# Optimization experiments

Hardware: AMD Instinct MI355X
Metric: run time of the kernel (lower is better)

The kernel has to match this reference:

```python
import jax, jax.numpy as jnp
import numpy as np

HEAD_SIZE = 1024
NUM_HEADS = 8
D_K = HEAD_SIZE // NUM_HEADS  # only used as the softmax scale; no head split in this module
B, S = 8, 2048


def setup_inputs() -> dict:
    key = jax.random.key(0)
    ks = jax.random.split(key, 11)
    d = HEAD_SIZE
    scale = 1.0 / np.sqrt(d)
    inp = {
        'query': jax.random.normal(ks[0], (B, S, d), dtype=jnp.float32),
        'key': jax.random.normal(ks[1], (B, S, d), dtype=jnp.float32),
        'value': jax.random.normal(ks[2], (B, S, d), dtype=jnp.float32),
        'Wq': jax.random.normal(ks[3], (d, d), dtype=jnp.float32) * scale,
        'bq': jnp.zeros((d,), dtype=jnp.float32),
        'Wk': jax.random.normal(ks[4], (d, d), dtype=jnp.float32) * scale,
        'bk': jnp.zeros((d,), dtype=jnp.float32),
        'Wv': jax.random.normal(ks[5], (d, d), dtype=jnp.float32) * scale,
        'bv': jnp.zeros((d,), dtype=jnp.float32),
        'Wo': jax.random.normal(ks[6], (d, d), dtype=jnp.float32) * scale,
        'bo': jnp.zeros((d,), dtype=jnp.float32),
    }
    return inp


def reference(query, key, value, Wq, bq, Wk, bk, Wv, bv, Wo, bo):
    # per-input linear projections (torch Linear: x @ W.T + b)
    q = jnp.einsum('bsd,ed->bse', query, Wq) + bq
    k = jnp.einsum('bsd,ed->bse', key, Wk) + bk
    v = jnp.einsum('bsd,ed->bse', value, Wv) + bv
    # NOTE: no head split in the original module; scale uses d_k = head_size/num_heads
    scores = jnp.einsum('bqd,bkd->bqk', q, k) / jnp.sqrt(jnp.float32(D_K))
    p_attn = jax.nn.softmax(scores, axis=-1)  # [B, S, S]
    x = jnp.einsum('bqk,bkd->bqd', p_attn, v)
    out = jnp.einsum('bsd,ed->bse', x, Wo) + bo
    return out
```

## Files before the change

### kernel.cpp

```cpp
#include <hip/hip_runtime.h>
#include <hip/hip_bf16.h>
#include <math.h>

typedef __bf16 bf16_t;
typedef _Float16 f16_t;
typedef bf16_t bf16x8 __attribute__((ext_vector_type(8)));
typedef bf16_t bf16x4 __attribute__((ext_vector_type(4)));
typedef f16_t  f16x8  __attribute__((ext_vector_type(8)));
typedef f16_t  f16x4  __attribute__((ext_vector_type(4)));
typedef float  f32x4  __attribute__((ext_vector_type(4)));

__global__ __launch_bounds__(256) void cvt_f32_bf16(
    const float* __restrict__ in, bf16_t* __restrict__ out, int n4) {
  int i = blockIdx.x * 256 + threadIdx.x;
  if (i >= n4) return;
  float4 v = ((const float4*)in)[i];
  bf16x4 o;
  o[0] = (bf16_t)v.x; o[1] = (bf16_t)v.y; o[2] = (bf16_t)v.z; o[3] = (bf16_t)v.w;
  ((bf16x4*)out)[i] = o;
}

__global__ __launch_bounds__(256) void transpose_bf16(
    const bf16_t* __restrict__ in, bf16_t* __restrict__ out, int R, int C) {
  __shared__ bf16_t t[64][65];
  size_t boff = (size_t)blockIdx.z * R * C;
  in += boff; out += boff;
  int r0 = blockIdx.y * 64, c0 = blockIdx.x * 64;
  int x = threadIdx.x & 63, y4 = threadIdx.x >> 6;
  #pragma unroll
  for (int yy = y4; yy < 64; yy += 4)
    t[yy][x] = in[(size_t)(r0 + yy) * C + c0 + x];
  __syncthreads();
  #pragma unroll
  for (int yy = y4; yy < 64; yy += 4)
    out[(size_t)(c0 + yy) * R + r0 + x] = t[x][yy];
}

__global__ __launch_bounds__(256) void softmax_rows_f16(f16_t* __restrict__ sc) {
  f16_t* rp = sc + (size_t)blockIdx.x * 2048;
  int tid = threadIdx.x;
  f16x8 v = ((const f16x8*)rp)[tid];
  float f[8];
  #pragma unroll
  for (int t = 0; t < 8; t++) f[t] = (float)v[t];

  float m = f[0];
  #pragma unroll
  for (int t = 1; t < 8; t++) m = fmaxf(m, f[t]);
  #pragma unroll
  for (int o = 32; o; o >>= 1) m = fmaxf(m, __shfl_xor(m, o));
  __shared__ float redm[4];
  if ((tid & 63) == 0) redm[tid >> 6] = m;
  __syncthreads();
  m = fmaxf(fmaxf(redm[0], redm[1]), fmaxf(redm[2], redm[3]));

  float s = 0.f;
  #pragma unroll
  for (int t = 0; t < 8; t++) { f[t] = __expf(f[t] - m); s += f[t]; }
  #pragma unroll
  for (int o = 32; o; o >>= 1) s += __shfl_xor(s, o);
  __shared__ float reds[4];
  if ((tid & 63) == 0) reds[tid >> 6] = s;
  __syncthreads();
  s = reds[0] + reds[1] + reds[2] + reds[3];
  float inv = 1.0f / s;

  bf16x8 o8;
  #pragma unroll
  for (int t = 0; t < 8; t++) o8[t] = (bf16_t)(f[t] * inv);
  ((bf16x8*)rp)[tid] = o8;
}

__device__ __forceinline__ void store4(float* p, float4 v) { *(float4*)p = v; }
__device__ __forceinline__ void store4(bf16_t* p, float4 v) {
  bf16x4 o; o[0] = (bf16_t)v.x; o[1] = (bf16_t)v.y;
  o[2] = (bf16_t)v.z; o[3] = (bf16_t)v.w; *(bf16x4*)p = o;
}
__device__ __forceinline__ void store4(f16_t* p, float4 v) {
  f16x4 o; o[0] = (f16_t)v.x; o[1] = (f16_t)v.y;
  o[2] = (f16_t)v.z; o[3] = (f16_t)v.w; *(f16x4*)p = o;
}

#define BM 256
#define BN 256
#define BK 64

__device__ __forceinline__ void load16_lds(const bf16_t* g, bf16_t* l) {
  __builtin_amdgcn_global_load_lds(
      (__attribute__((address_space(1))) void*)const_cast<bf16_t*>(g),
      (__attribute__((address_space(3))) void*)l, 16, 0, 0);
}

template <typename CT>
__global__ __launch_bounds__(512, 2) void gemm256(
    const bf16_t* __restrict__ A, int lda, size_t strA,
    const bf16_t* __restrict__ B, int ldb, size_t strB,
    CT* __restrict__ C, int ldc, size_t strC,
    const float* __restrict__ bias, float scale,
    int K, int batch_on_x) {
  __shared__ __align__(16) char smem[2][65536];

  int bz, mt, nt;
  if (batch_on_x) { bz = blockIdx.x; nt = blockIdx.y; mt = blockIdx.z; }
  else            { mt = blockIdx.x; nt = blockIdx.y; bz = blockIdx.z; }
  A += (size_t)bz * strA;
  B += (size_t)bz * strB;
  C += (size_t)bz * strC;
  int m0 = mt * BM, n0 = nt * BN;
  int tid  = threadIdx.x;
  int lane = tid & 63, wv = tid >> 6;
  int wrow = wv >> 2;
  int wcol = wv & 3;

  f32x4 acc[8][4];
  #pragma unroll
  for (int i = 0; i < 8; i++)
    #pragma unroll
    for (int j = 0; j < 4; j++) acc[i][j] = (f32x4)0.f;

  int lrow = lane & 15;
  int lk8  = (lane >> 4) * 8;
  int xm   = (lrow & 8) << 2;

  auto rd = [&](const char* base, int blk16, int kcol) -> bf16x8 {
    int byte = (((blk16 << 1) + (kcol >> 5)) << 10)
             + (lrow << 6) + (((kcol & 31) << 1) ^ xm);
    return *(const bf16x8*)(base + byte);
  };

  auto stage_half = [&](int h) {
    int th = h >> 2, hf = h & 3;
    char* dstb = smem[th & 1] + hf * 16384;
    const bf16_t* g; int rb, ld;
    if (hf < 2) { g = A; rb = m0 + hf * 128;       ld = lda; }
    else        { g = B; rb = n0 + (hf - 2) * 128; ld = ldb; }
    int k0 = th * BK;
    #pragma unroll
    for (int q = 0; q < 2; q++) {
      int l = q * 8192 + wv * 1024 + lane * 16;
      int inner = l & 1023, s = l >> 10;
      int rl   = ((s >> 1) << 4) | (inner >> 6);
      int colb = (inner & 63) ^ (((inner >> 9) & 1) << 5);
      int col  = ((s & 1) << 5) | (colb >> 1);
      load16_lds(g + (size_t)(rb + rl) * ld + k0 + col,
                 (bf16_t*)(dstb + q * 8192 + wv * 1024));
    }
  };

  int nk = K / BK;

  #pragma unroll
  for (int h = 0; h < 6; ++h)
    if (h < 4 * nk) stage_half(h);
  asm volatile("s_waitcnt vmcnt(4)" ::: "memory");
  asm volatile("s_barrier" ::: "memory");

  bf16x8 a0[4][2], a1[4][2], bb[2][2];

  for (int t = 0; t < nk; ++t) {
    const char* Ab = smem[t & 1];
    const char* Bb = smem[t & 1] + 32768;
    int hb = 4 * t + 6;

    #pragma unroll
    for (int i = 0; i < 4; ++i)
      #pragma unroll
      for (int s = 0; s < 2; ++s)
        a0[i][s] = rd(Ab, wrow * 8 + i, s * 32 + lk8);
    #pragma unroll
    for (int j = 0; j < 2; ++j)
      #pragma unroll
      for (int s = 0; s < 2; ++s)
        bb[j][s] = rd(Bb, wcol * 4 + j, s * 32 + lk8);
    if (hb + 0 < 4 * nk) stage_half(hb + 0);
    asm volatile("s_barrier" ::: "memory");
    asm volatile("s_waitcnt lgkmcnt(0)");
    __builtin_amdgcn_s_setprio(1);
    #pragma unroll
    for (int i = 0; i < 4; ++i)
      #pragma unroll
      for (int j = 0; j < 2; ++j)
        #pragma unroll
        for (int s = 0; s < 2; ++s)
          acc[i][j] = __builtin_amdgcn_mfma_f32_16x16x32_bf16(
              a0[i][s], bb[j][s], acc[i][j], 0, 0, 0);
    __builtin_amdgcn_s_setprio(0);
    asm volatile("s_barrier" ::: "memory");

    #pragma unroll
    for (int i = 0; i < 4; ++i)
      #pragma unroll
      for (int s = 0; s < 2; ++s)
        a1[i][s] = rd(Ab, wrow * 8 + 4 + i, s * 32 + lk8);
    if (hb + 1 < 4 * nk) stage_half(hb + 1);
    asm volatile("s_barrier" ::: "memory");
    asm volatile("s_waitcnt lgkmcnt(0)");
    __builtin_amdgcn_s_setprio(1);
    #pragma unroll
    for (int i = 0; i < 4; ++i)
      #pragma unroll
      for (int j = 0; j < 2; ++j)
        #pragma unroll
        for (int s = 0; s < 2; ++s)
          acc[4 + i][j] = __builtin_amdgcn_mfma_f32_16x16x32_bf16(
              a1[i][s], bb[j][s], acc[4 + i][j], 0, 0, 0);
    __builtin_amdgcn_s_setprio(0);
    asm volatile("s_barrier" ::: "memory");

    #pragma unroll
    for (int j = 0; j < 2; ++j)
      #pragma unroll
      for (int s = 0; s < 2; ++s)
        bb[j][s] = rd(Bb, wcol * 4 + 2 + j, s * 32 + lk8);
    if (hb + 2 < 4 * nk) stage_half(hb + 2);
    asm volatile("s_barrier" ::: "memory");
    asm volatile("s_waitcnt lgkmcnt(0)");
    __builtin_amdgcn_s_setprio(1);
    #pragma unroll
    for (int i = 0; i < 4; ++i)
      #pragma unroll
      for (int j = 0; j < 2; ++j)
        #pragma unroll
        for (int s = 0; s < 2; ++s)
          acc[4 + i][2 + j] = __builtin_amdgcn_mfma_f32_16x16x32_bf16(
              a1[i][s], bb[j][s], acc[4 + i][2 + j], 0, 0, 0);
    __builtin_amdgcn_s_setprio(0);
    asm volatile("s_barrier" ::: "memory");

    if (hb + 3 < 4 * nk) stage_half(hb + 3);
    asm volatile("s_barrier" ::: "memory");
    __builtin_amdgcn_s_setprio(1);
    #pragma unroll
    for (int i = 0; i < 4; ++i)
      #pragma unroll
      for (int j = 0; j < 2; ++j)
        #pragma unroll
        for (int s = 0; s < 2; ++s)
          acc[i][2 + j] = __builtin_amdgcn_mfma_f32_16x16x32_bf16(
              a0[i][s], bb[j][s], acc[i][2 + j], 0, 0, 0);
    __builtin_amdgcn_s_setprio(0);
    if (t < nk - 2) asm volatile("s_waitcnt vmcnt(4)" ::: "memory");
    else            asm volatile("s_waitcnt vmcnt(0)" ::: "memory");
    asm volatile("s_barrier" ::: "memory");
  }

  float* Cs = (float*)smem[0];
  #pragma unroll
  for (int q = 0; q < 4; ++q) {
    __syncthreads();
    if (wrow == (q >> 1)) {
      #pragma unroll
      for (int ii = 0; ii < 4; ++ii) {
        int i = (q & 1) * 4 + ii;
        int lr = ii * 16 + (lane >> 4) * 4;
        #pragma unroll
        for (int j = 0; j < 4; ++j) {
          int lc = wcol * 64 + j * 16 + (lane & 15);
          #pragma unroll
          for (int r = 0; r < 4; ++r)
            Cs[(lr + r) * 260 + lc] = acc[i][j][r];
        }
      }
    }
    __syncthreads();
    #pragma unroll
    for (int io = 0; io < 8; ++io) {
      int idx = io * 512 + tid;
      int r = idx >> 6, c4 = (idx & 63) * 4;
      float4 v = *(const float4*)&Cs[r * 260 + c4];
      int grow = m0 + q * 64 + r;
      int gcol = n0 + c4;
      float4 bv = bias ? *(const float4*)&bias[gcol] : make_float4(0, 0, 0, 0);
      v.x = v.x * scale + bv.x; v.y = v.y * scale + bv.y;
      v.z = v.z * scale + bv.z; v.w = v.w * scale + bv.w;
      store4(C + (size_t)grow * ldc + gcol, v);
    }
  }
}

extern "C" void kernel_launch(void* const* d_in, const int* in_sizes, int n_in,
                              void* d_out, int out_size, void* d_ws, size_t ws_size,
                              hipStream_t stream) {
  const float* query = (const float*)d_in[0];
  const float* key_  = (const float*)d_in[1];
  const float* value = (const float*)d_in[2];
  const float* Wq = (const float*)d_in[3];
  const float* bq = (const float*)d_in[4];
  const float* Wk = (const float*)d_in[5];
  const float* bk = (const float*)d_in[6];
  const float* Wv = (const float*)d_in[7];
  const float* bv = (const float*)d_in[8];
  const float* Wo = (const float*)d_in[9];
  const float* bo = (const float*)d_in[10];
  float* out = (float*)d_out;

  const int Bb = 8, S = 2048, D = 1024;
  const int MS = Bb * S;
  const size_t ND = (size_t)MS * D;
  const size_t WD = (size_t)D * D;

  char* ws = (char*)d_ws;
  bf16_t* Wqb = (bf16_t*)ws;
  bf16_t* Wkb = Wqb + WD;
  bf16_t* Wvb = Wkb + WD;
  bf16_t* Wob = Wvb + WD;
  f16_t*  SC  = (f16_t*)(Wob + WD);
  bf16_t* IN  = (bf16_t*)SC;
  bf16_t* Qb  = (bf16_t*)((char*)SC + (size_t)Bb * S * S * 2);
  bf16_t* Kb  = Qb + ND;
  bf16_t* VT  = Kb;
  bf16_t* Xb  = Kb + ND;

  const int n4i = (int)(ND / 4), n4w = (int)(WD / 4);
  dim3 blk(512);

  cvt_f32_bf16<<<dim3(n4w / 256), 256, 0, stream>>>(Wq, Wqb, n4w);
  cvt_f32_bf16<<<dim3(n4w / 256), 256, 0, stream>>>(Wk, Wkb, n4w);
  cvt_f32_bf16<<<dim3(n4w / 256), 256, 0, stream>>>(Wv, Wvb, n4w);
  cvt_f32_bf16<<<dim3(n4w / 256), 256, 0, stream>>>(Wo, Wob, n4w);

  dim3 pgrid(MS / BM, D / BN, 1);
  cvt_f32_bf16<<<dim3(n4i / 256), 256, 0, stream>>>(query, IN, n4i);
  gemm256<bf16_t><<<pgrid, blk, 0, stream>>>(
      IN, D, 0, Wqb, D, 0, Qb, D, 0, bq, 1.f, D, 0);
  cvt_f32_bf16<<<dim3(n4i / 256), 256, 0, stream>>>(key_, IN, n4i);
  gemm256<bf16_t><<<pgrid, blk, 0, stream>>>(
      IN, D, 0, Wkb, D, 0, Kb, D, 0, bk, 1.f, D, 0);
  cvt_f32_bf16<<<dim3(n4i / 256), 256, 0, stream>>>(value, IN, n4i);
  gemm256<bf16_t><<<pgrid, blk, 0, stream>>>(
      IN, D, 0, Wvb, D, 0, Xb, D, 0, bv, 1.f, D, 0);

  gemm256<f16_t><<<dim3(Bb, S / BN, S / BM), blk, 0, stream>>>(
      Qb, D, (size_t)S * D, Kb, D, (size_t)S * D, SC, S, (size_t)S * S,
      nullptr, 0.08838834764831845f, D, 1);

  transpose_bf16<<<dim3(D / 64, S / 64, Bb), 256, 0, stream>>>(Xb, VT, S, D);

  softmax_rows_f16<<<dim3(Bb * S), 256, 0, stream>>>(SC);

  gemm256<bf16_t><<<dim3(Bb, D / BN, S / BM), blk, 0, stream>>>(
      (const bf16_t*)SC, S, (size_t)S * S, VT, S, (size_t)D * S,
      Xb, D, (size_t)S * D, nullptr, 1.f, S, 1);

  gemm256<float><<<pgrid, blk, 0, stream>>>(
      Xb, D, 0, Wob, D, 0, out, D, 0, bo, 1.f, D, 0);
}
```

Baseline: 574.3 us.

## Replace double-buffered LDS with a 10-slot ring to deepen global prefetch

```diff
diff --git a/kernel.cpp b/kernel.cpp
--- a/kernel.cpp
+++ b/kernel.cpp
@@ -98,7 +98,8 @@
     CT* __restrict__ C, int ldc, size_t strC,
     const float* __restrict__ bias, float scale,
     int K, int batch_on_x) {
-  __shared__ __align__(16) char smem[2][65536];
+  __shared__ __align__(16) char smem[10][16384];
+  char* smem0 = &smem[0][0];
 
   int bz, mt, nt;
   if (batch_on_x) { bz = blockIdx.x; nt = blockIdx.y; mt = blockIdx.z; }
@@ -122,15 +123,15 @@
   int lk8  = (lane >> 4) * 8;
   int xm   = (lrow & 8) << 2;
 
-  auto rd = [&](const char* base, int blk16, int kcol) -> bf16x8 {
-    int byte = (((blk16 << 1) + (kcol >> 5)) << 10)
+  auto rd = [&](const char* half, int blk, int kcol) -> bf16x8 {
+    int byte = (((blk << 1) + (kcol >> 5)) << 10)
              + (lrow << 6) + (((kcol & 31) << 1) ^ xm);
-    return *(const bf16x8*)(base + byte);
+    return *(const bf16x8*)(half + byte);
   };
 
-  auto stage_half = [&](int h) {
+  auto stage_half = [&](int h, int slot) {
     int th = h >> 2, hf = h & 3;
-    char* dstb = smem[th & 1] + hf * 16384;
+    char* dstb = smem0 + slot * 16384;
     const bf16_t* g; int rb, ld;
     if (hf < 2) { g = A; rb = m0 + hf * 128;       ld = lda; }
     else        { g = B; rb = n0 + (hf - 2) * 128; ld = ldb; }
@@ -148,31 +149,37 @@
   };
 
   int nk = K / BK;
-
-  #pragma unroll
-  for (int h = 0; h < 6; ++h)
-    if (h < 4 * nk) stage_half(h);
-  asm volatile("s_waitcnt vmcnt(4)" ::: "memory");
+  int nh = 4 * nk;
+
+  #pragma unroll
+  for (int h = 0; h < 8; ++h)
+    if (h < nh) stage_half(h, h);
+  asm volatile("s_waitcnt vmcnt(8)" ::: "memory");
   asm volatile("s_barrier" ::: "memory");
 
   bf16x8 a0[4][2], a1[4][2], bb[2][2];
+  int rs = 0;
+  int ss = 8;
 
   for (int t = 0; t < nk; ++t) {
-    const char* Ab = smem[t & 1];
-    const char* Bb = smem[t & 1] + 32768;
-    int hb = 4 * t + 6;
+    int hb = 4 * t + 8;
+    int sa = rs + wrow;
+    int sb = rs + 2 + (wcol >> 1); if (sb >= 10) sb -= 10;
+    const char* Ah = smem0 + sa * 16384;
+    const char* Bh = smem0 + sb * 16384;
+    int bl = (wcol & 1) * 4;
 
     #pragma unroll
     for (int i = 0; i < 4; ++i)
       #pragma unroll
       for (int s = 0; s < 2; ++s)
-        a0[i][s] = rd(Ab, wrow * 8 + i, s * 32 + lk8);
+        a0[i][s] = rd(Ah, i, s * 32 + lk8);
     #pragma unroll
     for (int j = 0; j < 2; ++j)
       #pragma unroll
       for (int s = 0; s < 2; ++s)
-        bb[j][s] = rd(Bb, wcol * 4 + j, s * 32 + lk8);
-    if (hb + 0 < 4 * nk) stage_half(hb + 0);
+        bb[j][s] = rd(Bh, bl + j, s * 32 + lk8);
+    if (hb + 0 < nh) { stage_half(hb + 0, ss); ss = (ss == 9) ? 0 : ss + 1; }
     asm volatile("s_barrier" ::: "memory");
     asm volatile("s_waitcnt lgkmcnt(0)");
     __builtin_amdgcn_s_setprio(1);
@@ -191,8 +198,8 @@
     for (int i = 0; i < 4; ++i)
       #pragma unroll
       for (int s = 0; s < 2; ++s)
-        a1[i][s] = rd(Ab, wrow * 8 + 4 + i, s * 32 + lk8);
-    if (hb + 1 < 4 * nk) stage_half(hb + 1);
+        a1[i][s] = rd(Ah, 4 + i, s * 32 + lk8);
+    if (hb + 1 < nh) { stage_half(hb + 1, ss); ss = (ss == 9) ? 0 : ss + 1; }
     asm volatile("s_barrier" ::: "memory");
     asm volatile("s_waitcnt lgkmcnt(0)");
     __builtin_amdgcn_s_setprio(1);
@@ -211,8 +218,8 @@
     for (int j = 0; j < 2; ++j)
       #pragma unroll
       for (int s = 0; s < 2; ++s)
-        bb[j][s] = rd(Bb, wcol * 4 + 2 + j, s * 32 + lk8);
-    if (hb + 2 < 4 * nk) stage_half(hb + 2);
+        bb[j][s] = rd(Bh, bl + 2 + j, s * 32 + lk8);
+    if (hb + 2 < nh) { stage_half(hb + 2, ss); ss = (ss == 9) ? 0 : ss + 1; }
     asm volatile("s_barrier" ::: "memory");
     asm volatile("s_waitcnt lgkmcnt(0)");
     __builtin_amdgcn_s_setprio(1);
@@ -227,7 +234,7 @@
     __builtin_amdgcn_s_setprio(0);
     asm volatile("s_barrier" ::: "memory");
 
-    if (hb + 3 < 4 * nk) stage_half(hb + 3);
+    if (hb + 3 < nh) { stage_half(hb + 3, ss); ss = (ss == 9) ? 0 : ss + 1; }
     asm volatile("s_barrier" ::: "memory");
     __builtin_amdgcn_s_setprio(1);
     #pragma unroll
@@ -239,12 +246,14 @@
           acc[i][2 + j] = __builtin_amdgcn_mfma_f32_16x16x32_bf16(
               a0[i][s], bb[j][s], acc[i][2 + j], 0, 0, 0);
     __builtin_amdgcn_s_setprio(0);
-    if (t < nk - 2) asm volatile("s_waitcnt vmcnt(4)" ::: "memory");
+    if (t < nk - 2) asm volatile("s_waitcnt vmcnt(8)" ::: "memory");
     else            asm volatile("s_waitcnt vmcnt(0)" ::: "memory");
     asm volatile("s_barrier" ::: "memory");
+
+    rs += 4; if (rs >= 10) rs -= 10;
   }
 
-  float* Cs = (float*)smem[0];
+  float* Cs = (float*)smem0;
   #pragma unroll
   for (int q = 0; q < 4; ++q) {
     __syncthreads();
```

Result: no change. 579.4 us (+0.9%).
